# Performance work log

Hardware: AMD Instinct MI355X
Metric: run time of the kernel (lower is better)

The kernel has to match this reference:

```python
import jax, jax.numpy as jnp
import numpy as np

B, S, D, H = 2, 2048, 1024, 16
DK = D // H


def setup_inputs() -> dict:
    key = jax.random.key(0)
    ks = jax.random.split(key, 11)
    std = 1.0 / np.sqrt(D)
    inp = {
        "query": jax.random.normal(ks[0], (B, S, D), jnp.float32),
        "key": jax.random.normal(ks[1], (B, S, D), jnp.float32),
        "value": jax.random.normal(ks[2], (B, S, D), jnp.float32),
        # True = masked position (torch masked_fill semantics); causal mask
        "mask": jnp.triu(jnp.ones((1, 1, S, S), jnp.bool_), k=1),
        "Wq": jax.random.normal(ks[3], (D, D), jnp.float32) * std,
        "bq": jnp.zeros((D,), jnp.float32),
        "Wk": jax.random.normal(ks[4], (D, D), jnp.float32) * std,
        "bk": jnp.zeros((D,), jnp.float32),
        "Wv": jax.random.normal(ks[5], (D, D), jnp.float32) * std,
        "bv": jnp.zeros((D,), jnp.float32),
        "Wo": jax.random.normal(ks[6], (D, D), jnp.float32) * std,
        "bo": jnp.zeros((D,), jnp.float32),
    }
    return inp


def _split_heads(x):
    b, s, _ = x.shape
    return x.reshape(b, s, H, DK).transpose(0, 2, 1, 3)  # [b, H, s, dk]


def reference(query, key, value, mask, Wq, bq, Wk, bk, Wv, bv, Wo, bo):
    q = _split_heads(query @ Wq + bq)
    k = _split_heads(key @ Wk + bk)
    v = _split_heads(value @ Wv + bv)
    scale = 1.0 / (DK ** 0.5)
    logits = jnp.einsum("bhqd,bhkd->bhqk", q, k) * scale
    logits = jnp.where(mask, -1.0e9, logits)
    w = jax.nn.softmax(logits, axis=-1)
    att = jnp.einsum("bhqk,bhkd->bhqd", w, v)  # [B, H, S, dk]
    # NOTE: faithful to the original bug -- view() without permuting heads back,
    # i.e. a raw row-major reshape [B,H,S,dk] -> [B,S,H*dk].
    att = att.reshape(att.shape[0], att.shape[2], -1)
    out = att @ Wo + bo
    return out
```

## Files before the change

kernel.cpp:

```cpp
#include <hip/hip_runtime.h>
#include <hip/hip_bf16.h>

typedef __hip_bfloat16 bf16;
typedef __attribute__((ext_vector_type(8))) short bf16x8;
typedef __attribute__((ext_vector_type(4))) float f32x4;

constexpr int Bc  = 2;
constexpr int Sc  = 2048;
constexpr int Dc  = 1024;
constexpr int Hc  = 16;
constexpr int DKc = 64;

__device__ __forceinline__ float bfbits2f(unsigned short u) {
  return __uint_as_float(((unsigned)u) << 16);
}
__device__ __forceinline__ unsigned short f2bfbits(float x) {
  bf16 h = __float2bfloat16(x);
  return *reinterpret_cast<unsigned short*>(&h);
}
__device__ __forceinline__ void store1_dyn(char* base, size_t ei, int isf32, float v) {
  if (isf32) *reinterpret_cast<float*>(base + ei * 4) = v;
  else       *reinterpret_cast<bf16*>(base + ei * 2) = __float2bfloat16(v);
}
__device__ __forceinline__ float fast_exp2(float x) {
  return __builtin_amdgcn_exp2f(x);
}
__device__ __forceinline__ unsigned pkbf16(float a, float b) {
  __hip_bfloat162 h = __float22bfloat162_rn(make_float2(a, b));
  return *reinterpret_cast<unsigned*>(&h);
}
__device__ __forceinline__ uint4 pack8(const float4& a, const float4& b) {
  uint4 r;
  r.x = pkbf16(a.x, a.y);
  r.y = pkbf16(a.z, a.w);
  r.z = pkbf16(b.x, b.y);
  r.w = pkbf16(b.z, b.w);
  return r;
}
__device__ __forceinline__ void gld16(const void* g, void* l) {
  __builtin_amdgcn_global_load_lds(
      (const __attribute__((address_space(1))) unsigned int*)g,
      (__attribute__((address_space(3))) unsigned int*)l, 16, 0, 0);
}

__global__ void detect_dtype(const unsigned short* __restrict__ q, int* __restrict__ flag) {
  __shared__ int cnt[256];
  const int tid = threadIdx.x;
  int c = 0;
  for (int i = tid; i < 2048; i += 256) {
    const unsigned short u = q[i];
    const int e = (u >> 7) & 0xFF;
    if (e >= 134 || e <= 90) ++c;
  }
  cnt[tid] = c;
  __syncthreads();
  for (int s = 128; s > 0; s >>= 1) {
    if (tid < s) cnt[tid] += cnt[tid + s];
    __syncthreads();
  }
  if (tid == 0) flag[0] = (cnt[0] > 64) ? 1 : 0;
}

__global__ __launch_bounds__(256)
void prep_all(const char* __restrict__ W0, const char* __restrict__ W1,
              const char* __restrict__ W2, const char* __restrict__ W3,
              unsigned short* __restrict__ Wt_all,
              const char* __restrict__ b0, const char* __restrict__ b1,
              const char* __restrict__ b2, const char* __restrict__ b3,
              unsigned short* __restrict__ bb_all,
              const char* __restrict__ A0, const char* __restrict__ A1,
              const char* __restrict__ A2, bf16* __restrict__ B0,
              bf16* __restrict__ B1, bf16* __restrict__ B2,
              const int* __restrict__ flagp) {
  __shared__ unsigned short T[64][72];
  const int dyn = flagp[0];
  const int id = blockIdx.x;
  const int tid = threadIdx.x;

  if (id < 1024) {
    const int z = id >> 8, rem = id & 255;
    const int n0 = (rem & 15) * 64, k0 = (rem >> 4) * 64;
    const char* W = (z == 0) ? W0 : (z == 1) ? W1 : (z == 2) ? W2 : W3;
    unsigned short* Wt = Wt_all + (size_t)z * Dc * Dc;
    const int r = tid >> 2, c16 = (tid & 3) * 16;

    unsigned short us[16];
    if (dyn) {
      const float4* p = reinterpret_cast<const float4*>(
          W + ((size_t)(k0 + r) * Dc + n0 + c16) * 4);
      const float4 f0 = p[0], f1 = p[1], f2 = p[2], f3 = p[3];
      const float fv[16] = {f0.x, f0.y, f0.z, f0.w, f1.x, f1.y, f1.z, f1.w,
                            f2.x, f2.y, f2.z, f2.w, f3.x, f3.y, f3.z, f3.w};
#pragma unroll
      for (int i = 0; i < 16; ++i) us[i] = f2bfbits(fv[i]);
    } else {
      const ushort4* p = reinterpret_cast<const ushort4*>(
          W + ((size_t)(k0 + r) * Dc + n0 + c16) * 2);
      const ushort4 u0 = p[0], u1 = p[1], u2 = p[2], u3 = p[3];
      us[0] = u0.x;  us[1] = u0.y;  us[2] = u0.z;  us[3] = u0.w;
      us[4] = u1.x;  us[5] = u1.y;  us[6] = u1.z;  us[7] = u1.w;
      us[8] = u2.x;  us[9] = u2.y;  us[10] = u2.z; us[11] = u2.w;
      us[12] = u3.x; us[13] = u3.y; us[14] = u3.z; us[15] = u3.w;
    }
#pragma unroll
    for (int i = 0; i < 16; ++i) T[r][c16 + i] = us[i];
    __syncthreads();

    unsigned vs[8];
#pragma unroll
    for (int i = 0; i < 8; ++i)
      vs[i] = (unsigned)T[c16 + 2 * i][r] | ((unsigned)T[c16 + 2 * i + 1][r] << 16);
    uint4* op = reinterpret_cast<uint4*>(Wt + (size_t)(n0 + r) * Dc + k0 + c16);
    op[0] = make_uint4(vs[0], vs[1], vs[2], vs[3]);
    op[1] = make_uint4(vs[4], vs[5], vs[6], vs[7]);
  } else if (id < 2560) {
    const int j = id - 1024;
    const int z = j >> 9, x = j & 511;
    const char* src = (z == 0) ? A0 : (z == 1) ? A1 : A2;
    bf16* dst = (z == 0) ? B0 : (z == 1) ? B1 : B2;
    const size_t n = (size_t)4096 * Dc;
    const size_t stride = (size_t)512 * 256 * 8;
    for (size_t i = ((size_t)x * 256 + tid) * 8; i < n; i += stride) {
      uint4 u;
      if (dyn) {
        const float4* p = reinterpret_cast<const float4*>(src + i * 4);
        u = pack8(p[0], p[1]);
      } else {
        u = *reinterpret_cast<const uint4*>(src + i * 2);
      }
      *reinterpret_cast<uint4*>(dst + i) = u;
    }
  } else {
    const int x = id - 2560;
    const char* src = (x == 0) ? b0 : (x == 1) ? b1 : (x == 2) ? b2 : b3;
    for (int i = tid; i < Dc; i += 256) {
      float v = dyn ? reinterpret_cast<const float*>(src)[i]
                    : bfbits2f(reinterpret_cast<const unsigned short*>(src)[i]);
      bb_all[x * Dc + i] = f2bfbits(v);
    }
  }
}

__global__ __launch_bounds__(256)
void qkv_gemm_async(const bf16* __restrict__ A0, const bf16* __restrict__ A1,
                    const bf16* __restrict__ A2,
                    const unsigned short* __restrict__ Wt_all,
                    const unsigned short* __restrict__ bias_all,
                    bf16* __restrict__ C0, bf16* __restrict__ C1,
                    bf16* __restrict__ C2) {
  constexpr int K = Dc, N = Dc;
  __shared__ __align__(16) unsigned short At[128 * 32];
  __shared__ __align__(16) unsigned short Bt[128 * 32];

  const int z = blockIdx.z;
  const bf16* A = (z == 0) ? A0 : (z == 1) ? A1 : A2;
  bf16* C = (z == 0) ? C0 : (z == 1) ? C1 : C2;
  const float scale = (z == 0) ? 0.18033688011112042f : 1.0f;
  const unsigned short* Wt = Wt_all + (size_t)z * Dc * Dc;
  const unsigned short* bias = bias_all + z * Dc;

  const int tid = threadIdx.x;
  const int m0 = blockIdx.x * 128, n0 = blockIdx.y * 128;
  const int w = tid >> 6, lane = tid & 63;
  const int lo16 = lane & 15, quad = lane >> 4;
  const int wm = (w >> 1) * 64, wn = (w & 1) * 64;

  unsigned short* ldsA = &At[w * 1024 + lane * 8];
  unsigned short* ldsB = &Bt[w * 1024 + lane * 8];
  const bf16* gA = A + (size_t)(m0 + w * 32 + (lane >> 2)) * K + (lane & 3) * 8;
  const unsigned short* gB = Wt + (size_t)(n0 + w * 32 + (lane >> 2)) * K + (lane & 3) * 8;

  f32x4 acc[4][4] = {};

  for (int k0 = 0; k0 < K; k0 += 32) {
    gld16(gA + k0, ldsA);
    gld16(gA + (size_t)16 * K + k0, ldsA + 512);
    gld16(gB + k0, ldsB);
    gld16(gB + (size_t)16 * K + k0, ldsB + 512);
    __syncthreads();

    bf16x8 afr[4], bfr[4];
#pragma unroll
    for (int mt = 0; mt < 4; ++mt)
      afr[mt] = *reinterpret_cast<const bf16x8*>(&At[(wm + mt * 16 + lo16) * 32 + quad * 8]);
#pragma unroll
    for (int nt = 0; nt < 4; ++nt)
      bfr[nt] = *reinterpret_cast<const bf16x8*>(&Bt[(wn + nt * 16 + lo16) * 32 + quad * 8]);
#pragma unroll
    for (int mt = 0; mt < 4; ++mt)
#pragma unroll
      for (int nt = 0; nt < 4; ++nt)
        acc[mt][nt] = __builtin_amdgcn_mfma_f32_16x16x32_bf16(afr[mt], bfr[nt],
                                                              acc[mt][nt], 0, 0, 0);
    __syncthreads();
  }

  float bv[4];
#pragma unroll
  for (int nt = 0; nt < 4; ++nt)
    bv[nt] = bfbits2f(bias[n0 + wn + nt * 16 + lo16]);
#pragma unroll
  for (int mt = 0; mt < 4; ++mt)
#pragma unroll
    for (int r = 0; r < 4; ++r) {
      const int row = m0 + wm + mt * 16 + quad * 4 + r;
#pragma unroll
      for (int nt = 0; nt < 4; ++nt) {
        const int col = n0 + wn + nt * 16 + lo16;
        C[(size_t)row * N + col] = __float2bfloat16((acc[mt][nt][r] + bv[nt]) * scale);
      }
    }
}

__global__ __launch_bounds__(256)
void qkv_gemm(const char* __restrict__ A0, const char* __restrict__ A1,
              const char* __restrict__ A2, const unsigned short* __restrict__ Wt_all,
              const unsigned short* __restrict__ bias_all,
              bf16* __restrict__ C0, bf16* __restrict__ C1, bf16* __restrict__ C2,
              const int* __restrict__ flagp) {
  constexpr int K = Dc, N = Dc;
  __shared__ __align__(16) unsigned short At[128][32];
  __shared__ __align__(16) unsigned short Bt[128][32];

  const int z = blockIdx.z;
  const char* A = (z == 0) ? A0 : (z == 1) ? A1 : A2;
  bf16* C = (z == 0) ? C0 : (z == 1) ? C1 : C2;
  const float scale = (z == 0) ? 0.18033688011112042f : 1.0f;
  const unsigned short* Wt = Wt_all + (size_t)z * Dc * Dc;
  const unsigned short* bias = bias_all + z * Dc;
  const int af = flagp[0];

  const int tid = threadIdx.x;
  const int m0 = blockIdx.x * 128, n0 = blockIdx.y * 128;
  const int w = tid >> 6, lane = tid & 63;
  const int lo16 = lane & 15, quad = lane >> 4;
  const int wm = (w >> 1) * 64, wn = (w & 1) * 64;
  const int sr = tid >> 1, sh = (tid & 1) * 16;

  f32x4 acc[4][4] = {};

  for (int k0 = 0; k0 < K; k0 += 32) {
    uint4 a_lo, a_hi;
    if (af) {
      const float4* p = reinterpret_cast<const float4*>(
          A + ((size_t)(m0 + sr) * K + k0 + sh) * 4);
      a_lo = pack8(p[0], p[1]);
      a_hi = pack8(p[2], p[3]);
    } else {
      const uint4* p = reinterpret_cast<const uint4*>(
          A + ((size_t)(m0 + sr) * K + k0 + sh) * 2);
      a_lo = p[0];
      a_hi = p[1];
    }
    const uint4* wp = reinterpret_cast<const uint4*>(Wt + (size_t)(n0 + sr) * K + k0 + sh);
    const uint4 b_lo = wp[0], b_hi = wp[1];

    __syncthreads();
    *reinterpret_cast<uint4*>(&At[sr][sh])     = a_lo;
    *reinterpret_cast<uint4*>(&At[sr][sh + 8]) = a_hi;
    *reinterpret_cast<uint4*>(&Bt[sr][sh])     = b_lo;
    *reinterpret_cast<uint4*>(&Bt[sr][sh + 8]) = b_hi;
    __syncthreads();

    bf16x8 afr[4], bfr[4];
#pragma unroll
    for (int mt = 0; mt < 4; ++mt)
      afr[mt] = *reinterpret_cast<const bf16x8*>(&At[wm + mt * 16 + lo16][quad * 8]);
#pragma unroll
    for (int nt = 0; nt < 4; ++nt)
      bfr[nt] = *reinterpret_cast<const bf16x8*>(&Bt[wn + nt * 16 + lo16][quad * 8]);
#pragma unroll
    for (int mt = 0; mt < 4; ++mt)
#pragma unroll
      for (int nt = 0; nt < 4; ++nt)
        acc[mt][nt] = __builtin_amdgcn_mfma_f32_16x16x32_bf16(afr[mt], bfr[nt],
                                                              acc[mt][nt], 0, 0, 0);
  }

  float bv[4];
#pragma unroll
  for (int nt = 0; nt < 4; ++nt)
    bv[nt] = bfbits2f(bias[n0 + wn + nt * 16 + lo16]);
#pragma unroll
  for (int mt = 0; mt < 4; ++mt)
#pragma unroll
    for (int r = 0; r < 4; ++r) {
      const int row = m0 + wm + mt * 16 + quad * 4 + r;
#pragma unroll
      for (int nt = 0; nt < 4; ++nt) {
        const int col = n0 + wn + nt * 16 + lo16;
        C[(size_t)row * N + col] = __float2bfloat16((acc[mt][nt][r] + bv[nt]) * scale);
      }
    }
}

__global__ __launch_bounds__(256)
void out_gemm_async(const bf16* __restrict__ A, const unsigned short* __restrict__ Wt,
                    const unsigned short* __restrict__ bias, char* __restrict__ C,
                    const int* __restrict__ flagp) {
  constexpr int K = Dc, N = Dc;
  __shared__ __align__(16) unsigned short At[64 * 32];
  __shared__ __align__(16) unsigned short Bt[128 * 32];

  const int cf = flagp[0];
  const int tid = threadIdx.x;
  const int m0 = blockIdx.x * 64, n0 = blockIdx.y * 128;
  const int w = tid >> 6, lane = tid & 63;
  const int lo16 = lane & 15, quad = lane >> 4;
  const int wm = (w >> 1) * 32, wn = (w & 1) * 64;

  unsigned short* ldsA = &At[w * 512 + lane * 8];
  unsigned short* ldsB = &Bt[w * 1024 + lane * 8];
  const bf16* gA = A + (size_t)(m0 + w * 16 + (lane >> 2)) * K + (lane & 3) * 8;
  const unsigned short* gB = Wt + (size_t)(n0 + w * 32 + (lane >> 2)) * K + (lane & 3) * 8;

  f32x4 acc[2][4] = {};

  for (int k0 = 0; k0 < K; k0 += 32) {
    gld16(gA + k0, ldsA);
    gld16(gB + k0, ldsB);
    gld16(gB + (size_t)16 * K + k0, ldsB + 512);
    __syncthreads();

    bf16x8 afr[2], bfr[4];
#pragma unroll
    for (int mt = 0; mt < 2; ++mt)
      afr[mt] = *reinterpret_cast<const bf16x8*>(&At[(wm + mt * 16 + lo16) * 32 + quad * 8]);
#pragma unroll
    for (int nt = 0; nt < 4; ++nt)
      bfr[nt] = *reinterpret_cast<const bf16x8*>(&Bt[(wn + nt * 16 + lo16) * 32 + quad * 8]);
#pragma unroll
    for (int mt = 0; mt < 2; ++mt)
#pragma unroll
      for (int nt = 0; nt < 4; ++nt)
        acc[mt][nt] = __builtin_amdgcn_mfma_f32_16x16x32_bf16(afr[mt], bfr[nt],
                                                              acc[mt][nt], 0, 0, 0);
    __syncthreads();
  }

  float bv[4];
#pragma unroll
  for (int nt = 0; nt < 4; ++nt)
    bv[nt] = bfbits2f(bias[n0 + wn + nt * 16 + lo16]);
#pragma unroll
  for (int mt = 0; mt < 2; ++mt)
#pragma unroll
    for (int r = 0; r < 4; ++r) {
      const int row = m0 + wm + mt * 16 + quad * 4 + r;
#pragma unroll
      for (int nt = 0; nt < 4; ++nt) {
        const int col = n0 + wn + nt * 16 + lo16;
        store1_dyn(C, (size_t)row * N + col, cf, acc[mt][nt][r] + bv[nt]);
      }
    }
}

__global__ __launch_bounds__(256)
void attn_mfma(const bf16* __restrict__ Q, const bf16* __restrict__ K,
               const bf16* __restrict__ V, bf16* __restrict__ O) {
  __shared__ __align__(16) unsigned short Kt[64][72];
  __shared__ __align__(16) unsigned short Vt[64][72];
  __shared__ __align__(16) unsigned short St[4][16][72];
  __shared__ float Li[4][16];

  const int hb = blockIdx.x & 31;
  const int i  = blockIdx.x >> 5;
  const int g = i >> 3, r0 = i & 7;
  const int qt = (g == 0) ? r0 : (g == 1) ? 15 - r0 : (g == 2) ? 16 + r0 : 31 - r0;
  const int b = hb >> 4, h = hb & 15;
  const int q0 = qt * 64;
  const int tid = threadIdx.x;
  const int w = tid >> 6;
  const int lane = tid & 63;
  const int lo16 = lane & 15, quad = lane >> 4;
  const size_t hd = (size_t)h * DKc;

  const int kr = tid >> 2, kc = (tid & 3) * 16;
  const int vk = (tid & 31) * 2, vd0 = (tid >> 5) * 8;

  const bf16* qrow = Q + ((size_t)(b * Sc + q0 + w * 16 + lo16)) * Dc + hd;
  const bf16x8 qa0 = *reinterpret_cast<const bf16x8*>(qrow + quad * 8);
  const bf16x8 qa1 = *reinterpret_cast<const bf16x8*>(qrow + 32 + quad * 8);

  f32x4 oacc[4] = {f32x4{0,0,0,0}, f32x4{0,0,0,0}, f32x4{0,0,0,0}, f32x4{0,0,0,0}};
  float lsum = 0.f;
  const int qg = q0 + w * 16 + lo16;

  for (int t = 0; t <= qt; ++t) {
    const int kt = t * 64;
    __syncthreads();
    {
      const bf16* kp = K + ((size_t)(b * Sc + kt + kr)) * Dc + hd + kc;
      const uint4 k0v = *reinterpret_cast<const uint4*>(kp);
      const uint4 k1v = *reinterpret_cast<const uint4*>(kp + 8);
      *reinterpret_cast<uint4*>(&Kt[kr][kc])     = k0v;
      *reinterpret_cast<uint4*>(&Kt[kr][kc + 8]) = k1v;
    }
    {
      const bf16* vbase = V + ((size_t)(b * Sc + kt + vk)) * Dc + hd + vd0;
      const uint4 ra = *reinterpret_cast<const uint4*>(vbase);
      const uint4 rb = *reinterpret_cast<const uint4*>(vbase + Dc);
      *reinterpret_cast<unsigned*>(&Vt[vd0 + 0][vk]) = (ra.x & 0xffffu) | (rb.x << 16);
      *reinterpret_cast<unsigned*>(&Vt[vd0 + 1][vk]) = (ra.x >> 16)     | (rb.x & 0xffff0000u);
      *reinterpret_cast<unsigned*>(&Vt[vd0 + 2][vk]) = (ra.y & 0xffffu) | (rb.y << 16);
      *reinterpret_cast<unsigned*>(&Vt[vd0 + 3][vk]) = (ra.y >> 16)     | (rb.y & 0xffff0000u);
      *reinterpret_cast<unsigned*>(&Vt[vd0 + 4][vk]) = (ra.z & 0xffffu) | (rb.z << 16);
      *reinterpret_cast<unsigned*>(&Vt[vd0 + 5][vk]) = (ra.z >> 16)     | (rb.z & 0xffff0000u);
      *reinterpret_cast<unsigned*>(&Vt[vd0 + 6][vk]) = (ra.w & 0xffffu) | (rb.w << 16);
      *reinterpret_cast<unsigned*>(&Vt[vd0 + 7][vk]) = (ra.w >> 16)     | (rb.w & 0xffff0000u);
    }
    __syncthreads();

    f32x4 s[4] = {f32x4{0,0,0,0}, f32x4{0,0,0,0}, f32x4{0,0,0,0}, f32x4{0,0,0,0}};
#pragma unroll
    for (int ct = 0; ct < 4; ++ct) {
      const bf16x8 ka0 = *reinterpret_cast<const bf16x8*>(&Kt[ct * 16 + lo16][quad * 8]);
      const bf16x8 ka1 = *reinterpret_cast<const bf16x8*>(&Kt[ct * 16 + lo16][32 + quad * 8]);
      s[ct] = __builtin_amdgcn_mfma_f32_16x16x32_bf16(ka0, qa0, s[ct], 0, 0, 0);
      s[ct] = __builtin_amdgcn_mfma_f32_16x16x32_bf16(ka1, qa1, s[ct], 0, 0, 0);
    }

    if (kt + 63 > q0 + w * 16) {
#pragma unroll
      for (int ct = 0; ct < 4; ++ct)
#pragma unroll
        for (int r = 0; r < 4; ++r)
          if (kt + ct * 16 + quad * 4 + r > qg) s[ct][r] = -1e9f;
    }

#pragma unroll
    for (int ct = 0; ct < 4; ++ct) {
      const float p0 = fast_exp2(s[ct][0]);
      const float p1 = fast_exp2(s[ct][1]);
      const float p2 = fast_exp2(s[ct][2]);
      const float p3 = fast_exp2(s[ct][3]);
      lsum += (p0 + p1) + (p2 + p3);
      uint2 pk;
      pk.x = pkbf16(p0, p1);
      pk.y = pkbf16(p2, p3);
      *reinterpret_cast<uint2*>(&St[w][lo16][ct * 16 + quad * 4]) = pk;
    }

    const bf16x8 pa0 = *reinterpret_cast<const bf16x8*>(&St[w][lo16][quad * 8]);
    const bf16x8 pa1 = *reinterpret_cast<const bf16x8*>(&St[w][lo16][32 + quad * 8]);
#pragma unroll
    for (int ct = 0; ct < 4; ++ct) {
      const bf16x8 vb0 = *reinterpret_cast<const bf16x8*>(&Vt[ct * 16 + lo16][quad * 8]);
      const bf16x8 vb1 = *reinterpret_cast<const bf16x8*>(&Vt[ct * 16 + lo16][32 + quad * 8]);
      oacc[ct] = __builtin_amdgcn_mfma_f32_16x16x32_bf16(pa0, vb0, oacc[ct], 0, 0, 0);
      oacc[ct] = __builtin_amdgcn_mfma_f32_16x16x32_bf16(pa1, vb1, oacc[ct], 0, 0, 0);
    }
  }

  lsum += __shfl_xor(lsum, 16);
  lsum += __shfl_xor(lsum, 32);
  if (quad == 0) Li[w][lo16] = 1.f / lsum;
  __builtin_amdgcn_wave_barrier();
  const f32x4 invv = *reinterpret_cast<const f32x4*>(&Li[w][quad * 4]);

#pragma unroll
  for (int r = 0; r < 4; ++r) {
    bf16* op = O + (((size_t)(b * Hc + h) * Sc) + q0 + w * 16 + quad * 4 + r) * DKc + lo16;
#pragma unroll
    for (int ct = 0; ct < 4; ++ct)
      op[ct * 16] = __float2bfloat16(oacc[ct][r] * invv[r]);
  }
}

extern "C" void kernel_launch(void* const* d_in, const int* in_sizes, int n_in,
                              void* d_out, int out_size, void* d_ws, size_t ws_size,
                              hipStream_t stream) {
  (void)in_sizes; (void)out_size;
  const char* query = (const char*)d_in[0];
  const char* key_  = (const char*)d_in[1];
  const char* value = (const char*)d_in[2];
  const int wb = n_in - 8;
  const char* Wq = (const char*)d_in[wb + 0];
  const char* bq = (const char*)d_in[wb + 1];
  const char* Wk = (const char*)d_in[wb + 2];
  const char* bk = (const char*)d_in[wb + 3];
  const char* Wv = (const char*)d_in[wb + 4];
  const char* bv = (const char*)d_in[wb + 5];
  const char* Wo = (const char*)d_in[wb + 6];
  const char* bo = (const char*)d_in[wb + 7];

  char* ws = (char*)d_ws;
  bf16* Qs  = (bf16*)(ws);
  bf16* Ks  = (bf16*)(ws + ((size_t)8  << 20));
  bf16* Vs  = (bf16*)(ws + ((size_t)16 << 20));
  bf16* att = (bf16*)(ws + ((size_t)24 << 20));
  unsigned short* Wt_all = (unsigned short*)(ws + ((size_t)32 << 20));
  unsigned short* bb_all = (unsigned short*)(ws + ((size_t)40 << 20));
  int* flag = (int*)(ws + ((size_t)40 << 20) + 16384);
  bf16* Qb = (bf16*)(ws + ((size_t)42 << 20));
  bf16* Kb = (bf16*)(ws + ((size_t)50 << 20));
  bf16* Vb = (bf16*)(ws + ((size_t)58 << 20));
  const bool big_ws = ws_size >= ((size_t)66 << 20);

  detect_dtype<<<1, 256, 0, stream>>>((const unsigned short*)query, flag);

  if (big_ws) {
    prep_all<<<2564, 256, 0, stream>>>(Wq, Wk, Wv, Wo, Wt_all, bq, bk, bv, bo,
                                       bb_all, query, key_, value, Qb, Kb, Vb, flag);
    qkv_gemm_async<<<dim3(32, 8, 3), 256, 0, stream>>>(Qb, Kb, Vb, Wt_all, bb_all,
                                                       Qs, Ks, Vs);
  } else {
    prep_all<<<1028, 256, 0, stream>>>(Wq, Wk, Wv, Wo, Wt_all, bq, bk, bv, bo,
                                       bb_all, query, key_, value,
                                       (bf16*)att, (bf16*)att, (bf16*)att, flag);
    qkv_gemm<<<dim3(32, 8, 3), 256, 0, stream>>>(query, key_, value, Wt_all, bb_all,
                                                 Qs, Ks, Vs, flag);
  }

  attn_mfma<<<dim3(1024), 256, 0, stream>>>(Qs, Ks, Vs, att);

  out_gemm_async<<<dim3(64, 8), 256, 0, stream>>>(att, Wt_all + (size_t)3 * Dc * Dc,
                                                  bb_all + 3 * Dc, (char*)d_out, flag);
}
```

Before: 236.3 us.

## Enlarge attention blocks to 128 queries with register-prefetched, role-split K/V loads

The attention kernel now uses 512-thread blocks covering 128 query rows, so each K/V tile loaded into shared memory is reused by eight waves instead of four, and the grid is halved. The K and V tile loads are split between the two halves of the block and prefetched into registers one iteration ahead, which overlaps global loads with compute. Waves whose rows are fully masked for a tile skip its compute. MFMA sections are wrapped in s_setprio to favour matrix issue. This adds register pressure and a larger block, which may lower occupancy, and waves skipping causal tiles still sit idle at the barriers.

Result: no change. 239.7 us (+1.4%).

```diff
diff --git a/kernel.cpp b/kernel.cpp
--- a/kernel.cpp
+++ b/kernel.cpp
@@ -355,28 +355,30 @@
     }
 }
 
-__global__ __launch_bounds__(256)
+__global__ __launch_bounds__(512)
 void attn_mfma(const bf16* __restrict__ Q, const bf16* __restrict__ K,
                const bf16* __restrict__ V, bf16* __restrict__ O) {
   __shared__ __align__(16) unsigned short Kt[64][72];
   __shared__ __align__(16) unsigned short Vt[64][72];
-  __shared__ __align__(16) unsigned short St[4][16][72];
-  __shared__ float Li[4][16];
+  __shared__ __align__(16) unsigned short St[8][16][72];
+  __shared__ float Li[8][16];
 
   const int hb = blockIdx.x & 31;
   const int i  = blockIdx.x >> 5;
   const int g = i >> 3, r0 = i & 7;
-  const int qt = (g == 0) ? r0 : (g == 1) ? 15 - r0 : (g == 2) ? 16 + r0 : 31 - r0;
+  const int c = g ? (15 - r0) : r0;
   const int b = hb >> 4, h = hb & 15;
-  const int q0 = qt * 64;
+  const int q0 = c * 128;
   const int tid = threadIdx.x;
   const int w = tid >> 6;
   const int lane = tid & 63;
   const int lo16 = lane & 15, quad = lane >> 4;
   const size_t hd = (size_t)h * DKc;
 
-  const int kr = tid >> 2, kc = (tid & 3) * 16;
-  const int vk = (tid & 31) * 2, vd0 = (tid >> 5) * 8;
+  const int t256 = tid & 255;
+  const int kr = t256 >> 2, kc = (t256 & 3) * 16;
+  const int vk = (t256 & 31) * 2, vd0 = (t256 >> 5) * 8;
+  const bool vrole = (w < 4);
 
   const bf16* qrow = Q + ((size_t)(b * Sc + q0 + w * 16 + lo16)) * Dc + hd;
   const bf16x8 qa0 = *reinterpret_cast<const bf16x8*>(qrow + quad * 8);
@@ -384,34 +386,55 @@
 
   f32x4 oacc[4] = {f32x4{0,0,0,0}, f32x4{0,0,0,0}, f32x4{0,0,0,0}, f32x4{0,0,0,0}};
   float lsum = 0.f;
-  const int qg = q0 + w * 16 + lo16;
-
-  for (int t = 0; t <= qt; ++t) {
+  const int qg  = q0 + w * 16 + lo16;
+  const int qwm = q0 + w * 16 + 15;
+  const int nt = 2 * (c + 1);
+
+  const bf16* vsrc = V + ((size_t)(b * Sc + vk)) * Dc + hd + vd0;
+  const bf16* ksrc = K + ((size_t)(b * Sc + kr)) * Dc + hd + kc;
+
+  uint4 rA, rB;
+  if (vrole) {
+    rA = *reinterpret_cast<const uint4*>(vsrc);
+    rB = *reinterpret_cast<const uint4*>(vsrc + Dc);
+  } else {
+    rA = *reinterpret_cast<const uint4*>(ksrc);
+    rB = *reinterpret_cast<const uint4*>(ksrc + 8);
+  }
+
+  for (int t = 0; t < nt; ++t) {
     const int kt = t * 64;
     __syncthreads();
-    {
-      const bf16* kp = K + ((size_t)(b * Sc + kt + kr)) * Dc + hd + kc;
-      const uint4 k0v = *reinterpret_cast<const uint4*>(kp);
-      const uint4 k1v = *reinterpret_cast<const uint4*>(kp + 8);
-      *reinterpret_cast<uint4*>(&Kt[kr][kc])     = k0v;
-      *reinterpret_cast<uint4*>(&Kt[kr][kc + 8]) = k1v;
-    }
-    {
-      const bf16* vbase = V + ((size_t)(b * Sc + kt + vk)) * Dc + hd + vd0;
-      const uint4 ra = *reinterpret_cast<const uint4*>(vbase);
-      const uint4 rb = *reinterpret_cast<const uint4*>(vbase + Dc);
-      *reinterpret_cast<unsigned*>(&Vt[vd0 + 0][vk]) = (ra.x & 0xffffu) | (rb.x << 16);
-      *reinterpret_cast<unsigned*>(&Vt[vd0 + 1][vk]) = (ra.x >> 16)     | (rb.x & 0xffff0000u);
-      *reinterpret_cast<unsigned*>(&Vt[vd0 + 2][vk]) = (ra.y & 0xffffu) | (rb.y << 16);
-      *reinterpret_cast<unsigned*>(&Vt[vd0 + 3][vk]) = (ra.y >> 16)     | (rb.y & 0xffff0000u);
-      *reinterpret_cast<unsigned*>(&Vt[vd0 + 4][vk]) = (ra.z & 0xffffu) | (rb.z << 16);
-      *reinterpret_cast<unsigned*>(&Vt[vd0 + 5][vk]) = (ra.z >> 16)     | (rb.z & 0xffff0000u);
-      *reinterpret_cast<unsigned*>(&Vt[vd0 + 6][vk]) = (ra.w & 0xffffu) | (rb.w << 16);
-      *reinterpret_cast<unsigned*>(&Vt[vd0 + 7][vk]) = (ra.w >> 16)     | (rb.w & 0xffff0000u);
-    }
-    __syncthreads();
+    if (vrole) {
+      *reinterpret_cast<unsigned*>(&Vt[vd0 + 0][vk]) = (rA.x & 0xffffu) | (rB.x << 16);
+      *reinterpret_cast<unsigned*>(&Vt[vd0 + 1][vk]) = (rA.x >> 16)     | (rB.x & 0xffff0000u);
+      *reinterpret_cast<unsigned*>(&Vt[vd0 + 2][vk]) = (rA.y & 0xffffu) | (rB.y << 16);
+      *reinterpret_cast<unsigned*>(&Vt[vd0 + 3][vk]) = (rA.y >> 16)     | (rB.y & 0xffff0000u);
+      *reinterpret_cast<unsigned*>(&Vt[vd0 + 4][vk]) = (rA.z & 0xffffu) | (rB.z << 16);
+      *reinterpret_cast<unsigned*>(&Vt[vd0 + 5][vk]) = (rA.z >> 16)     | (rB.z & 0xffff0000u);
+      *reinterpret_cast<unsigned*>(&Vt[vd0 + 6][vk]) = (rA.w & 0xffffu) | (rB.w << 16);
+      *reinterpret_cast<unsigned*>(&Vt[vd0 + 7][vk]) = (rA.w >> 16)     | (rB.w & 0xffff0000u);
+    } else {
+      *reinterpret_cast<uint4*>(&Kt[kr][kc])     = rA;
+      *reinterpret_cast<uint4*>(&Kt[kr][kc + 8]) = rB;
+    }
+    __syncthreads();
+
+    if (t + 1 < nt) {
+      const size_t off = (size_t)(kt + 64) * Dc;
+      if (vrole) {
+        rA = *reinterpret_cast<const uint4*>(vsrc + off);
+        rB = *reinterpret_cast<const uint4*>(vsrc + off + Dc);
+      } else {
+        rA = *reinterpret_cast<const uint4*>(ksrc + off);
+        rB = *reinterpret_cast<const uint4*>(ksrc + off + 8);
+      }
+    }
+
+    if (kt > qwm) continue;
 
     f32x4 s[4] = {f32x4{0,0,0,0}, f32x4{0,0,0,0}, f32x4{0,0,0,0}, f32x4{0,0,0,0}};
+    __builtin_amdgcn_s_setprio(1);
 #pragma unroll
     for (int ct = 0; ct < 4; ++ct) {
       const bf16x8 ka0 = *reinterpret_cast<const bf16x8*>(&Kt[ct * 16 + lo16][quad * 8]);
@@ -419,6 +442,7 @@
       s[ct] = __builtin_amdgcn_mfma_f32_16x16x32_bf16(ka0, qa0, s[ct], 0, 0, 0);
       s[ct] = __builtin_amdgcn_mfma_f32_16x16x32_bf16(ka1, qa1, s[ct], 0, 0, 0);
     }
+    __builtin_amdgcn_s_setprio(0);
 
     if (kt + 63 > q0 + w * 16) {
 #pragma unroll
@@ -443,6 +467,7 @@
 
     const bf16x8 pa0 = *reinterpret_cast<const bf16x8*>(&St[w][lo16][quad * 8]);
     const bf16x8 pa1 = *reinterpret_cast<const bf16x8*>(&St[w][lo16][32 + quad * 8]);
+    __builtin_amdgcn_s_setprio(1);
 #pragma unroll
     for (int ct = 0; ct < 4; ++ct) {
       const bf16x8 vb0 = *reinterpret_cast<const bf16x8*>(&Vt[ct * 16 + lo16][quad * 8]);
@@ -450,6 +475,7 @@
       oacc[ct] = __builtin_amdgcn_mfma_f32_16x16x32_bf16(pa0, vb0, oacc[ct], 0, 0, 0);
       oacc[ct] = __builtin_amdgcn_mfma_f32_16x16x32_bf16(pa1, vb1, oacc[ct], 0, 0, 0);
     }
+    __builtin_amdgcn_s_setprio(0);
   }
 
   lsum += __shfl_xor(lsum, 16);
@@ -512,7 +538,7 @@
                                                  Qs, Ks, Vs, flag);
   }
 
-  attn_mfma<<<dim3(1024), 256, 0, stream>>>(Qs, Ks, Vs, att);
+  attn_mfma<<<dim3(512), 512, 0, stream>>>(Qs, Ks, Vs, att);
 
   out_gemm_async<<<dim3(64, 8), 256, 0, stream>>>(att, Wt_all + (size_t)3 * Dc * Dc,
                                                   bb_all + 3 * Dc, (char*)d_out, flag);
```
